# Optimization experiments

Measured on AMD Instinct MI355X. Metric: run time of the kernel, lower is better.

## Reference

```python
import jax, jax.numpy as jnp
import numpy as np

TOP_K = 2


def setup_inputs() -> dict:
    key = jax.random.key(0)
    ks = jax.random.split(key, 6)
    B, T, H, E, F = 2, 2048, 1024, 8, 4096
    s1 = 1.0 / np.sqrt(H)
    s2 = 1.0 / np.sqrt(F)
    return {
        "hidden_states": jax.random.normal(ks[0], (B, T, H), dtype=jnp.float32),
        "router_w": jax.random.normal(ks[1], (E, H), dtype=jnp.float32) * s1,
        "w1": jax.random.normal(ks[2], (E, H, F), dtype=jnp.float32) * s1,
        "b1": jnp.zeros((E, F), dtype=jnp.float32),
        "w2": jax.random.normal(ks[3], (E, F, H), dtype=jnp.float32) * s2,
        "b2": jnp.zeros((E, H), dtype=jnp.float32),
    }


def reference(hidden_states, router_w, w1, b1, w2, b2):
    # hidden_states: [B,T,H]; router_w: [E,H]; w1: [E,H,F]; w2: [E,F,H]
    E = router_w.shape[0]
    K = TOP_K
    dt = hidden_states.dtype

    # Router
    router_logits = jnp.einsum("bth,eh->bte", hidden_states, router_w)  # [B,T,E]
    topk_values, topk_indices = jax.lax.top_k(router_logits, K)         # [B,T,K]
    topk_weights = jax.nn.softmax(topk_values.astype(jnp.float32), axis=-1).astype(dt)

    # Dense all-expert MLP (module computes every expert on every token)
    h_mid = jax.nn.gelu(
        jnp.einsum("bth,ehf->btef", hidden_states, w1) + b1, approximate=False
    )  # [B,T,E,F]
    expert_outputs = jnp.einsum("btef,efh->bteh", h_mid, w2) + b2  # [B,T,E,H]

    # Gather top-K expert outputs and combine
    topk_out = jnp.take_along_axis(expert_outputs, topk_indices[..., None], axis=2)  # [B,T,K,H]
    mixed_output = jnp.sum(topk_out * topk_weights[..., None], axis=2)  # [B,T,H]

    # Load-balancing aux loss
    router_probs = jax.nn.softmax(router_logits.astype(jnp.float32), axis=-1)
    P = router_probs.mean(axis=(0, 1))                       # [E]
    hard = jax.nn.one_hot(topk_indices, E, dtype=jnp.float32)  # [B,T,K,E]
    f = hard.mean(axis=(0, 1, 2))                            # [E]
    aux_loss = jnp.float32(E) * jnp.sum(f * P)

    # concept_mat is None in a fresh module -> statement loss is exactly 0
    statement_loss = jnp.float32(0.0)
    return mixed_output, aux_loss, statement_loss
```

## Files before the change

### kernel.cpp

```cpp
#include <hip/hip_runtime.h>


typedef unsigned short ushort_t;
typedef __attribute__((ext_vector_type(2))) float f32x2;
typedef __attribute__((ext_vector_type(4))) unsigned int u32x4;
typedef __attribute__((ext_vector_type(4))) unsigned short u16x4;
typedef __attribute__((ext_vector_type(4))) float f32x4;
typedef __attribute__((ext_vector_type(8))) __bf16 bf16x8;

#define NTOK 4096
#define HD   1024
#define FD   4096
#define NE   8
#define NKTOT 8192

__device__ __forceinline__ ushort_t f2bf(float f) {
  unsigned u = __builtin_bit_cast(unsigned, f);
  u += 0x7fffu + ((u >> 16) & 1u);
  return (ushort_t)(u >> 16);
}
__device__ __forceinline__ unsigned pk2(float a, float b) {
  unsigned r;
  asm("v_cvt_pk_bf16_f32 %0, %1, %2" : "=v"(r) : "v"(a), "v"(b));
  return r;
}
__device__ __forceinline__ float bf2f(ushort_t u) {
  unsigned v = ((unsigned)u) << 16;
  return __builtin_bit_cast(float, v);
}
__device__ __forceinline__ bf16x8 frag_ld(const void* p) {
  u32x4 v = *reinterpret_cast<const u32x4*>(p);
  return __builtin_bit_cast(bf16x8, v);
}

#define GLOAD16(g, l) __builtin_amdgcn_global_load_lds(                         \
    (const __attribute__((address_space(1))) unsigned int*)(g),                 \
    (__attribute__((address_space(3))) unsigned int*)(l), 16, 0, 0)

#define WAITLGKM() do { asm volatile("s_waitcnt lgkmcnt(0)" ::: "memory");      \
                        __builtin_amdgcn_sched_barrier(0); } while (0)
#define WAITVM0()  asm volatile("s_waitcnt vmcnt(0)" ::: "memory")
#define BARRIER() do { asm volatile("s_waitcnt lgkmcnt(0)" ::: "memory");       \
                       __builtin_amdgcn_s_barrier(); } while (0)

__global__ void init_k(int* counts) {
  if (threadIdx.x < NE) counts[threadIdx.x] = 0;
}

__global__ void convx_k(const float* __restrict__ src, ushort_t* __restrict__ dst) {
  const size_t i = ((size_t)blockIdx.x * 256 + threadIdx.x) * 4;
  const f32x4 v = *reinterpret_cast<const f32x4*>(src + i);
  u16x4 o;
  o.x = f2bf(v.x); o.y = f2bf(v.y); o.z = f2bf(v.z); o.w = f2bf(v.w);
  *reinterpret_cast<u16x4*>(dst + i) = o;
}

__global__ void router_k(const float* __restrict__ x, const float* __restrict__ rw,
                         float* __restrict__ tokP, int* __restrict__ counts,
                         int* __restrict__ tk_e, int* __restrict__ tk_s,
                         float* __restrict__ tk_w) {
  const int w = threadIdx.x >> 6, l = threadIdx.x & 63;
  const int t = blockIdx.x * 4 + w;
  const float* xr = x + (size_t)t * HD;
  float acc[NE];
#pragma unroll
  for (int e = 0; e < NE; ++e) acc[e] = 0.f;
  for (int it = 0; it < HD / 64; ++it) {
    const int h = l + it * 64;
    const float xv = xr[h];
#pragma unroll
    for (int e = 0; e < NE; ++e) acc[e] = fmaf(xv, rw[e * HD + h], acc[e]);
  }
#pragma unroll
  for (int e = 0; e < NE; ++e) {
#pragma unroll
    for (int s = 32; s > 0; s >>= 1) acc[e] += __shfl_xor(acc[e], s, 64);
  }
  float m = acc[0];
#pragma unroll
  for (int e = 1; e < NE; ++e) m = fmaxf(m, acc[e]);
  float ssum = 0.f;
  float p[NE];
#pragma unroll
  for (int e = 0; e < NE; ++e) { p[e] = expf(acc[e] - m); ssum += p[e]; }
  const float inv = 1.f / ssum;
  if (l < NE) tokP[(size_t)t * NE + l] = p[l] * inv;

  if (l == 0) {
    int i0 = 0; float v0 = acc[0];
#pragma unroll
    for (int e = 1; e < NE; ++e) if (acc[e] > v0) { v0 = acc[e]; i0 = e; }
    int i1 = -1; float v1 = -3.4e38f;
#pragma unroll
    for (int e = 0; e < NE; ++e) if (e != i0 && acc[e] > v1) { v1 = acc[e]; i1 = e; }
    const float w0 = 1.f / (1.f + expf(v1 - v0));
    const int s0 = atomicAdd(&counts[i0], 1);
    const int s1 = atomicAdd(&counts[i1], 1);
    tk_e[2 * t] = i0;     tk_s[2 * t] = s0;     tk_w[2 * t] = w0;
    tk_e[2 * t + 1] = i1; tk_s[2 * t + 1] = s1; tk_w[2 * t + 1] = 1.f - w0;
  }
}

__global__ void finalize_k(const float* __restrict__ tokP, const int* __restrict__ counts,
                           int* __restrict__ offsets, float* __restrict__ out_tail) {
  __shared__ float red[16][8];
  const int tid = threadIdx.x;
  f32x4 a0 = {0.f, 0.f, 0.f, 0.f}, a1 = {0.f, 0.f, 0.f, 0.f};
#pragma unroll
  for (int k = 0; k < 4; ++k) {
    const float* p = tokP + ((size_t)tid * 4 + k) * 8;
    a0 += *reinterpret_cast<const f32x4*>(p);
    a1 += *reinterpret_cast<const f32x4*>(p + 4);
  }
#pragma unroll
  for (int s = 1; s < 64; s <<= 1) {
#pragma unroll
    for (int c = 0; c < 4; ++c) {
      a0[c] += __shfl_xor(a0[c], s, 64);
      a1[c] += __shfl_xor(a1[c], s, 64);
    }
  }
  if ((tid & 63) == 0) {
    const int wv = tid >> 6;
#pragma unroll
    for (int c = 0; c < 4; ++c) { red[wv][c] = a0[c]; red[wv][4 + c] = a1[c]; }
  }
  __syncthreads();
  if (tid == 0) {
    float P[8];
    for (int c = 0; c < 8; ++c) {
      float s = 0.f;
      for (int q = 0; q < 16; ++q) s += red[q][c];
      P[c] = s * (1.f / NTOK);
    }
    int off = 0; float aux = 0.f;
    for (int q = 0; q < NE; ++q) { offsets[q] = off; off += counts[q]; }
    for (int q = 0; q < NE; ++q) aux += ((float)counts[q] / (float)NKTOT) * P[q];
    out_tail[0] = (float)NE * aux;
    out_tail[1] = 0.f;
  }
}

__global__ void build_slots_k(const int* __restrict__ tk_e, const int* __restrict__ tk_s,
                              const int* __restrict__ offsets, int* __restrict__ slot_token) {
  const int i = blockIdx.x * 256 + threadIdx.x;
  const int e = tk_e[i];
  slot_token[offsets[e] + tk_s[i]] = i >> 1;
}

template <bool IS_G1>
__global__ __launch_bounds__(256, 4) void moe_fused(
    const ushort_t* __restrict__ A, const float* __restrict__ W,
    const float* __restrict__ bias,
    const int* __restrict__ counts, const int* __restrict__ offsets,
    const int* __restrict__ slot_token,
    ushort_t* __restrict__ midout, ushort_t* __restrict__ ybuf) {
  constexpr int KDF = IS_G1 ? HD : FD;
  constexpr int WST = IS_G1 ? FD : HD;
  constexpr int NSTEP = IS_G1 ? 16 : 32;
  const int id = blockIdx.x;
  const int e = id & 7;
  const int q = id >> 3;
  const int ty = q % 10;
  const int r = q / 10;
  const int np = IS_G1 ? r : (r >> 1);
  const int ks = IS_G1 ? 0 : (r & 1);
  const int n0 = np * 128;
  const int KB = ks * 2048;
  const int cnt = counts[e];
  if (ty * 128 >= cnt) return;
  const int off = offsets[e];
  const int pos0 = off + ty * 128;
  const int rr = cnt - ty * 128;
  const int rows_rem = rr < 128 ? rr : 128;

  __shared__ __align__(16) ushort_t lds[16384];

  const int tid = threadIdx.x;
  const int w = tid >> 6, l = tid & 63;
  const int wr = w >> 1, wc = w & 1;

  const int sw = (((l & 7) ^ ((l >> 3) & 7)) << 4);
  const char* ab[4];
#pragma unroll
  for (int c = 0; c < 4; ++c) {
    const int row = c * 32 + w * 8 + (l >> 3);
    int pos = pos0 + row; if (pos > NKTOT - 1) pos = NKTOT - 1;
    const size_t ar = IS_G1 ? (size_t)slot_token[pos] : (size_t)pos;
    ab[c] = (const char*)A + (ar * KDF + KB) * 2 + sw;
  }

  const float* wB = W + (size_t)e * ((size_t)HD * FD) +
                    ((size_t)KB + 16 * w) * WST + n0 + 2 * l;

  f32x4 acc[4][4] = {};

  for (int t = 0; t < NSTEP; ++t) {
#pragma unroll
    for (int c = 0; c < 4; ++c)
      GLOAD16(ab[c] + t * 128, &lds[(c * 32 + w * 8) * 64]);
    f32x2 R[16];
    const float* p = wB + (size_t)(t * 64) * WST;
#pragma unroll
    for (int i = 0; i < 16; ++i)
      R[i] = *reinterpret_cast<const f32x2*>(p + (size_t)i * WST);
    WAITVM0();
    {
      ushort_t* d = &lds[8192 + (2 * l) * 64];
      const int k7 = l & 7;
      u32x4 v;
      v.x = pk2(R[0].x, R[1].x); v.y = pk2(R[2].x, R[3].x);
      v.z = pk2(R[4].x, R[5].x); v.w = pk2(R[6].x, R[7].x);
      *reinterpret_cast<u32x4*>(d + (((2 * w) ^ k7) << 3)) = v;
      v.x = pk2(R[8].x, R[9].x);  v.y = pk2(R[10].x, R[11].x);
      v.z = pk2(R[12].x, R[13].x); v.w = pk2(R[14].x, R[15].x);
      *reinterpret_cast<u32x4*>(d + (((2 * w + 1) ^ k7) << 3)) = v;
      ushort_t* d2 = d + 64;
      v.x = pk2(R[0].y, R[1].y); v.y = pk2(R[2].y, R[3].y);
      v.z = pk2(R[4].y, R[5].y); v.w = pk2(R[6].y, R[7].y);
      *reinterpret_cast<u32x4*>(d2 + (((2 * w) ^ k7) << 3)) = v;
      v.x = pk2(R[8].y, R[9].y);  v.y = pk2(R[10].y, R[11].y);
      v.z = pk2(R[12].y, R[13].y); v.w = pk2(R[14].y, R[15].y);
      *reinterpret_cast<u32x4*>(d2 + (((2 * w + 1) ^ k7) << 3)) = v;
    }
    BARRIER();
    {
      const int arow = wr * 64 + (l & 15);
      const int brow = wc * 64 + (l & 15);
      const int ax = l & 7;
      const int bx = (l >> 1) & 7;
      bf16x8 afr[4], bfr[4];
#pragma unroll
      for (int kk = 0; kk < 2; ++kk) {
        const int kc = kk * 4 + (l >> 4);
#pragma unroll
        for (int mm = 0; mm < 4; ++mm)
          afr[mm] = frag_ld(&lds[(arow + mm * 16) * 64 + ((kc ^ ax) << 3)]);
#pragma unroll
        for (int nn = 0; nn < 4; ++nn)
          bfr[nn] = frag_ld(&lds[8192 + (brow + nn * 16) * 64 + ((kc ^ bx) << 3)]);
        WAITLGKM();
        __builtin_amdgcn_s_setprio(1);
#pragma unroll
        for (int mm = 0; mm < 4; ++mm)
#pragma unroll
          for (int nn = 0; nn < 4; ++nn)
            acc[mm][nn] = __builtin_amdgcn_mfma_f32_16x16x32_bf16(
                afr[mm], bfr[nn], acc[mm][nn], 0, 0, 0);
        __builtin_amdgcn_s_setprio(0);
      }
    }
    BARRIER();
  }

  {
    const int lr4 = (l >> 4) * 4, lc = l & 15;
#pragma unroll
    for (int nn = 0; nn < 4; ++nn) {
      const int col = wc * 64 + nn * 16 + lc;
      const float bv = IS_G1 ? bias[(size_t)e * FD + n0 + col] : 0.f;
#pragma unroll
      for (int mm = 0; mm < 4; ++mm) {
        const int rb = wr * 64 + mm * 16 + lr4;
#pragma unroll
        for (int j = 0; j < 4; ++j) {
          float v = acc[mm][nn][j] + bv;
          if (IS_G1) v = 0.5f * v * (1.0f + erff(v * 0.70710678118654752f));
          lds[(rb + j) * 128 + col] = f2bf(v);
        }
      }
    }
    BARRIER();
#pragma unroll
    for (int p = 0; p < 8; ++p) {
      const int idx = p * 2048 + tid * 8;
      const int row = idx >> 7;
      const int col = idx & 127;
      if (row < rows_rem) {
        const u32x4 v = *reinterpret_cast<const u32x4*>(&lds[idx]);
        if (IS_G1)
          *reinterpret_cast<u32x4*>(&midout[(size_t)(pos0 + row) * FD + n0 + col]) = v;
        else
          *reinterpret_cast<u32x4*>(
              &ybuf[((size_t)ks * NKTOT + pos0 + row) * HD + n0 + col]) = v;
      }
    }
  }
}

__global__ void combine_k(const ushort_t* __restrict__ ybuf, const int* __restrict__ tk_e,
                          const int* __restrict__ tk_s, const float* __restrict__ tk_w,
                          const int* __restrict__ offsets, const float* __restrict__ b2,
                          float* __restrict__ out) {
  const int t = blockIdx.x;
  const int e0 = tk_e[2 * t], e1 = tk_e[2 * t + 1];
  const size_t p0 = (size_t)offsets[e0] + tk_s[2 * t];
  const size_t p1 = (size_t)offsets[e1] + tk_s[2 * t + 1];
  const float w0 = tk_w[2 * t], w1v = tk_w[2 * t + 1];
  const int h = threadIdx.x * 4;
  f32x4 s0 = *reinterpret_cast<const f32x4*>(b2 + (size_t)e0 * HD + h);
  f32x4 s1 = *reinterpret_cast<const f32x4*>(b2 + (size_t)e1 * HD + h);
#pragma unroll
  for (int ks = 0; ks < 2; ++ks) {
    const u16x4 a = *reinterpret_cast<const u16x4*>(
        &ybuf[((size_t)ks * NKTOT + p0) * HD + h]);
    const u16x4 b = *reinterpret_cast<const u16x4*>(
        &ybuf[((size_t)ks * NKTOT + p1) * HD + h]);
    s0.x += bf2f(a.x); s0.y += bf2f(a.y); s0.z += bf2f(a.z); s0.w += bf2f(a.w);
    s1.x += bf2f(b.x); s1.y += bf2f(b.y); s1.z += bf2f(b.z); s1.w += bf2f(b.w);
  }
  f32x4 o = s0 * w0 + s1 * w1v;
  *reinterpret_cast<f32x4*>(out + (size_t)t * HD + h) = o;
}

extern "C" void kernel_launch(void* const* d_in, const int* in_sizes, int n_in,
                              void* d_out, int out_size, void* d_ws, size_t ws_size,
                              hipStream_t stream) {
  const float* x  = (const float*)d_in[0];
  const float* rw = (const float*)d_in[1];
  const float* w1 = (const float*)d_in[2];
  const float* b1 = (const float*)d_in[3];
  const float* w2 = (const float*)d_in[4];
  const float* b2 = (const float*)d_in[5];
  float* out = (float*)d_out;

  char* ws = (char*)d_ws;
  ushort_t* Xbf  = (ushort_t*)(ws + 0);
  ushort_t* midb = (ushort_t*)(ws + 8388608);
  ushort_t* ybuf = (ushort_t*)(ws + 75497472);
  char* sm = ws + 209715200;
  int*   counts  = (int*)(sm);
  int*   offsets = (int*)(sm + 64);
  float* tokP    = (float*)(sm + 128);
  int*   tk_e    = (int*)(sm + 128 + 131072);
  int*   tk_s    = (int*)(sm + 128 + 131072 + 32768);
  float* tk_w    = (float*)(sm + 128 + 131072 + 65536);
  int*   slot_token = (int*)(sm + 128 + 131072 + 98304);

  init_k<<<1, 64, 0, stream>>>(counts);
  convx_k<<<4096, 256, 0, stream>>>(x, Xbf);
  router_k<<<1024, 256, 0, stream>>>(x, rw, tokP, counts, tk_e, tk_s, tk_w);
  finalize_k<<<1, 1024, 0, stream>>>(tokP, counts, offsets, out + (size_t)NTOK * HD);
  build_slots_k<<<32, 256, 0, stream>>>(tk_e, tk_s, offsets, slot_token);
  moe_fused<true><<<2560, 256, 0, stream>>>(
      Xbf, w1, b1, counts, offsets, slot_token, midb, (ushort_t*)nullptr);
  moe_fused<false><<<1280, 256, 0, stream>>>(
      midb, w2, b2, counts, offsets, slot_token, (ushort_t*)nullptr, ybuf);
  combine_k<<<4096, 256, 0, stream>>>(ybuf, tk_e, tk_s, tk_w, offsets, b2, out);
}
```

Measured before the change: 463.3 us.

## Double-buffer A tiles and prefetch next K-step in larger 256-row expert GEMM blocks

Raises the expert GEMM block to 512 threads covering 256 token rows by 128 columns, which halves the grid and doubles reuse of each converted fp32 weight tile. The A tile is double-buffered in LDS, and the next step's A copy (global_load_lds) and weight register loads are issued before the MFMA compute of the current step. This overlaps memory latency with matrix math instead of stalling on vmcnt(0) each iteration. In exchange, LDS use grows to 80KB per block, which limits blocks per CU. Grouped experts with fewer tokens also waste more rows in partially filled 256-row tiles.

```diff
diff --git a/kernel.cpp b/kernel.cpp
--- a/kernel.cpp
+++ b/kernel.cpp
@@ -37,8 +37,7 @@
     (const __attribute__((address_space(1))) unsigned int*)(g),                 \
     (__attribute__((address_space(3))) unsigned int*)(l), 16, 0, 0)
 
-#define WAITLGKM() do { asm volatile("s_waitcnt lgkmcnt(0)" ::: "memory");      \
-                        __builtin_amdgcn_sched_barrier(0); } while (0)
+#define WAITVM4()  asm volatile("s_waitcnt vmcnt(4)" ::: "memory")
 #define WAITVM0()  asm volatile("s_waitcnt vmcnt(0)" ::: "memory")
 #define BARRIER() do { asm volatile("s_waitcnt lgkmcnt(0)" ::: "memory");       \
                        __builtin_amdgcn_s_barrier(); } while (0)
@@ -149,7 +148,7 @@
 }
 
 template <bool IS_G1>
-__global__ __launch_bounds__(256, 4) void moe_fused(
+__global__ __launch_bounds__(512, 4) void moe_fused(
     const ushort_t* __restrict__ A, const float* __restrict__ W,
     const float* __restrict__ bias,
     const int* __restrict__ counts, const int* __restrict__ offsets,
@@ -161,20 +160,20 @@
   const int id = blockIdx.x;
   const int e = id & 7;
   const int q = id >> 3;
-  const int ty = q % 10;
-  const int r = q / 10;
+  const int ty = q % 5;
+  const int r = q / 5;
   const int np = IS_G1 ? r : (r >> 1);
   const int ks = IS_G1 ? 0 : (r & 1);
   const int n0 = np * 128;
   const int KB = ks * 2048;
   const int cnt = counts[e];
-  if (ty * 128 >= cnt) return;
+  if (ty * 256 >= cnt) return;
   const int off = offsets[e];
-  const int pos0 = off + ty * 128;
-  const int rr = cnt - ty * 128;
-  const int rows_rem = rr < 128 ? rr : 128;
-
-  __shared__ __align__(16) ushort_t lds[16384];
+  const int pos0 = off + ty * 256;
+  const int rr = cnt - ty * 256;
+  const int rows_rem = rr < 256 ? rr : 256;
+
+  __shared__ __align__(16) ushort_t lds[40960];
 
   const int tid = threadIdx.x;
   const int w = tid >> 6, l = tid & 63;
@@ -184,74 +183,87 @@
   const char* ab[4];
 #pragma unroll
   for (int c = 0; c < 4; ++c) {
-    const int row = c * 32 + w * 8 + (l >> 3);
+    const int row = c * 64 + w * 8 + (l >> 3);
     int pos = pos0 + row; if (pos > NKTOT - 1) pos = NKTOT - 1;
     const size_t ar = IS_G1 ? (size_t)slot_token[pos] : (size_t)pos;
     ab[c] = (const char*)A + (ar * KDF + KB) * 2 + sw;
   }
 
   const float* wB = W + (size_t)e * ((size_t)HD * FD) +
-                    ((size_t)KB + 16 * w) * WST + n0 + 2 * l;
+                    ((size_t)KB + 8 * w) * WST + n0 + 2 * l;
 
   f32x4 acc[4][4] = {};
-
-  for (int t = 0; t < NSTEP; ++t) {
+  f32x2 R[8];
+
+  auto stageA = [&](int tt) {
+    const int bb = tt & 1;
 #pragma unroll
     for (int c = 0; c < 4; ++c)
-      GLOAD16(ab[c] + t * 128, &lds[(c * 32 + w * 8) * 64]);
-    f32x2 R[16];
-    const float* p = wB + (size_t)(t * 64) * WST;
-#pragma unroll
-    for (int i = 0; i < 16; ++i)
+      GLOAD16(ab[c] + tt * 128, &lds[bb * 16384 + (c * 64 + w * 8) * 64]);
+  };
+  auto issueB = [&](int tt) {
+    const float* p = wB + (size_t)tt * 64 * WST;
+#pragma unroll
+    for (int i = 0; i < 8; ++i)
       R[i] = *reinterpret_cast<const f32x2*>(p + (size_t)i * WST);
+  };
+  auto writeB = [&]() {
+    ushort_t* d = &lds[32768 + (2 * l) * 64 + ((w ^ (l & 7)) << 3)];
+    u32x4 v;
+    v.x = pk2(R[0].x, R[1].x); v.y = pk2(R[2].x, R[3].x);
+    v.z = pk2(R[4].x, R[5].x); v.w = pk2(R[6].x, R[7].x);
+    *reinterpret_cast<u32x4*>(d) = v;
+    v.x = pk2(R[0].y, R[1].y); v.y = pk2(R[2].y, R[3].y);
+    v.z = pk2(R[4].y, R[5].y); v.w = pk2(R[6].y, R[7].y);
+    *reinterpret_cast<u32x4*>(d + 64) = v;
+  };
+  auto compute = [&](int tt) {
+    const ushort_t* Ab = &lds[(tt & 1) * 16384];
+    const ushort_t* Bb = &lds[32768];
+    const int arow = wr * 64 + (l & 15);
+    const int brow = wc * 64 + (l & 15);
+    const int ax = l & 7;
+    const int bx = (l >> 1) & 7;
+    __builtin_amdgcn_s_setprio(1);
+#pragma unroll
+    for (int kk = 0; kk < 2; ++kk) {
+      const int kc = kk * 4 + (l >> 4);
+      bf16x8 afr[4];
+#pragma unroll
+      for (int mm = 0; mm < 4; ++mm)
+        afr[mm] = frag_ld(&Ab[(arow + mm * 16) * 64 + ((kc ^ ax) << 3)]);
+#pragma unroll
+      for (int nn = 0; nn < 4; ++nn) {
+        const bf16x8 bfr = frag_ld(&Bb[(brow + nn * 16) * 64 + ((kc ^ bx) << 3)]);
+#pragma unroll
+        for (int mm = 0; mm < 4; ++mm)
+          acc[mm][nn] = __builtin_amdgcn_mfma_f32_16x16x32_bf16(
+              afr[mm], bfr, acc[mm][nn], 0, 0, 0);
+      }
+    }
+    __builtin_amdgcn_s_setprio(0);
+  };
+
+  issueB(0);
+  stageA(0);
+  WAITVM4();
+  writeB();
+  WAITVM0();
+  BARRIER();
+
+  for (int t = 0; t < NSTEP - 1; ++t) {
+    issueB(t + 1);
+    stageA(t + 1);
+    __builtin_amdgcn_sched_barrier(0);
+    compute(t);
+    __builtin_amdgcn_s_barrier();
+    WAITVM4();
+    writeB();
     WAITVM0();
-    {
-      ushort_t* d = &lds[8192 + (2 * l) * 64];
-      const int k7 = l & 7;
-      u32x4 v;
-      v.x = pk2(R[0].x, R[1].x); v.y = pk2(R[2].x, R[3].x);
-      v.z = pk2(R[4].x, R[5].x); v.w = pk2(R[6].x, R[7].x);
-      *reinterpret_cast<u32x4*>(d + (((2 * w) ^ k7) << 3)) = v;
-      v.x = pk2(R[8].x, R[9].x);  v.y = pk2(R[10].x, R[11].x);
-      v.z = pk2(R[12].x, R[13].x); v.w = pk2(R[14].x, R[15].x);
-      *reinterpret_cast<u32x4*>(d + (((2 * w + 1) ^ k7) << 3)) = v;
-      ushort_t* d2 = d + 64;
-      v.x = pk2(R[0].y, R[1].y); v.y = pk2(R[2].y, R[3].y);
-      v.z = pk2(R[4].y, R[5].y); v.w = pk2(R[6].y, R[7].y);
-      *reinterpret_cast<u32x4*>(d2 + (((2 * w) ^ k7) << 3)) = v;
-      v.x = pk2(R[8].y, R[9].y);  v.y = pk2(R[10].y, R[11].y);
-      v.z = pk2(R[12].y, R[13].y); v.w = pk2(R[14].y, R[15].y);
-      *reinterpret_cast<u32x4*>(d2 + (((2 * w + 1) ^ k7) << 3)) = v;
-    }
     BARRIER();
-    {
-      const int arow = wr * 64 + (l & 15);
-      const int brow = wc * 64 + (l & 15);
-      const int ax = l & 7;
-      const int bx = (l >> 1) & 7;
-      bf16x8 afr[4], bfr[4];
-#pragma unroll
-      for (int kk = 0; kk < 2; ++kk) {
-        const int kc = kk * 4 + (l >> 4);
-#pragma unroll
-        for (int mm = 0; mm < 4; ++mm)
-          afr[mm] = frag_ld(&lds[(arow + mm * 16) * 64 + ((kc ^ ax) << 3)]);
-#pragma unroll
-        for (int nn = 0; nn < 4; ++nn)
-          bfr[nn] = frag_ld(&lds[8192 + (brow + nn * 16) * 64 + ((kc ^ bx) << 3)]);
-        WAITLGKM();
-        __builtin_amdgcn_s_setprio(1);
-#pragma unroll
-        for (int mm = 0; mm < 4; ++mm)
-#pragma unroll
-          for (int nn = 0; nn < 4; ++nn)
-            acc[mm][nn] = __builtin_amdgcn_mfma_f32_16x16x32_bf16(
-                afr[mm], bfr[nn], acc[mm][nn], 0, 0, 0);
-        __builtin_amdgcn_s_setprio(0);
-      }
-    }
-    BARRIER();
-  }
+  }
+  compute(NSTEP - 1);
+  __builtin_amdgcn_s_barrier();
 
   {
     const int lr4 = (l >> 4) * 4, lc = l & 15;
@@ -273,7 +285,7 @@
     BARRIER();
 #pragma unroll
     for (int p = 0; p < 8; ++p) {
-      const int idx = p * 2048 + tid * 8;
+      const int idx = p * 4096 + tid * 8;
       const int row = idx >> 7;
       const int col = idx & 127;
       if (row < rows_rem) {
@@ -342,9 +354,9 @@
   router_k<<<1024, 256, 0, stream>>>(x, rw, tokP, counts, tk_e, tk_s, tk_w);
   finalize_k<<<1, 1024, 0, stream>>>(tokP, counts, offsets, out + (size_t)NTOK * HD);
   build_slots_k<<<32, 256, 0, stream>>>(tk_e, tk_s, offsets, slot_token);
-  moe_fused<true><<<2560, 256, 0, stream>>>(
+  moe_fused<true><<<1280, 512, 0, stream>>>(
       Xbf, w1, b1, counts, offsets, slot_token, midb, (ushort_t*)nullptr);
-  moe_fused<false><<<1280, 256, 0, stream>>>(
+  moe_fused<false><<<640, 512, 0, stream>>>(
       midb, w2, b2, counts, offsets, slot_token, (ushort_t*)nullptr, ybuf);
   combine_k<<<4096, 256, 0, stream>>>(ybuf, tk_e, tk_s, tk_w, offsets, b2, out);
 }
```

New measurement: 397.8 us. 14.1% less time.

## Software-pipeline MoE GEMM loads, raise second-GEMM split-K, fuse bf16 cast into router

Applied to the files above, without the earlier changes.

Restructures the expert GEMM main loop as a multi-stage pipeline. Activation tiles are triple-buffered in LDS. Weight tiles are prefetched two steps ahead into alternating register sets, with partial vmcnt waits, and double-buffered in LDS. This is meant to hide global-load latency behind MFMA work. The second GEMM's split-K goes from 2 to 4 with twice as many blocks, and combine_k now sums four partials. The separate fp32-to-bf16 conversion kernel is folded into the router pass. The larger LDS footprint and the occupancy hint dropped to 2 blocks per CU reduce concurrency. The extra split-K partials add more ybuf traffic in combine.

```diff
diff --git a/kernel.cpp b/kernel.cpp
--- a/kernel.cpp
+++ b/kernel.cpp
@@ -37,9 +37,7 @@
     (const __attribute__((address_space(1))) unsigned int*)(g),                 \
     (__attribute__((address_space(3))) unsigned int*)(l), 16, 0, 0)
 
-#define WAITLGKM() do { asm volatile("s_waitcnt lgkmcnt(0)" ::: "memory");      \
-                        __builtin_amdgcn_sched_barrier(0); } while (0)
-#define WAITVM0()  asm volatile("s_waitcnt vmcnt(0)" ::: "memory")
+#define WAITVM(N) asm volatile("s_waitcnt vmcnt(" #N ")" ::: "memory")
 #define BARRIER() do { asm volatile("s_waitcnt lgkmcnt(0)" ::: "memory");       \
                        __builtin_amdgcn_s_barrier(); } while (0)
 
@@ -47,27 +45,22 @@
   if (threadIdx.x < NE) counts[threadIdx.x] = 0;
 }
 
-__global__ void convx_k(const float* __restrict__ src, ushort_t* __restrict__ dst) {
-  const size_t i = ((size_t)blockIdx.x * 256 + threadIdx.x) * 4;
-  const f32x4 v = *reinterpret_cast<const f32x4*>(src + i);
-  u16x4 o;
-  o.x = f2bf(v.x); o.y = f2bf(v.y); o.z = f2bf(v.z); o.w = f2bf(v.w);
-  *reinterpret_cast<u16x4*>(dst + i) = o;
-}
-
 __global__ void router_k(const float* __restrict__ x, const float* __restrict__ rw,
+                         ushort_t* __restrict__ Xbf,
                          float* __restrict__ tokP, int* __restrict__ counts,
                          int* __restrict__ tk_e, int* __restrict__ tk_s,
                          float* __restrict__ tk_w) {
   const int w = threadIdx.x >> 6, l = threadIdx.x & 63;
   const int t = blockIdx.x * 4 + w;
   const float* xr = x + (size_t)t * HD;
+  ushort_t* xo = Xbf + (size_t)t * HD;
   float acc[NE];
 #pragma unroll
   for (int e = 0; e < NE; ++e) acc[e] = 0.f;
   for (int it = 0; it < HD / 64; ++it) {
     const int h = l + it * 64;
     const float xv = xr[h];
+    xo[h] = f2bf(xv);
 #pragma unroll
     for (int e = 0; e < NE; ++e) acc[e] = fmaf(xv, rw[e * HD + h], acc[e]);
   }
@@ -149,7 +142,7 @@
 }
 
 template <bool IS_G1>
-__global__ __launch_bounds__(256, 4) void moe_fused(
+__global__ __launch_bounds__(256, 2) void moe_fused(
     const ushort_t* __restrict__ A, const float* __restrict__ W,
     const float* __restrict__ bias,
     const int* __restrict__ counts, const int* __restrict__ offsets,
@@ -157,16 +150,15 @@
     ushort_t* __restrict__ midout, ushort_t* __restrict__ ybuf) {
   constexpr int KDF = IS_G1 ? HD : FD;
   constexpr int WST = IS_G1 ? FD : HD;
-  constexpr int NSTEP = IS_G1 ? 16 : 32;
   const int id = blockIdx.x;
   const int e = id & 7;
   const int q = id >> 3;
   const int ty = q % 10;
   const int r = q / 10;
-  const int np = IS_G1 ? r : (r >> 1);
-  const int ks = IS_G1 ? 0 : (r & 1);
+  const int np = IS_G1 ? r : (r >> 2);
+  const int ks = IS_G1 ? 0 : (r & 3);
   const int n0 = np * 128;
-  const int KB = ks * 2048;
+  const int KB = ks * 1024;
   const int cnt = counts[e];
   if (ty * 128 >= cnt) return;
   const int off = offsets[e];
@@ -174,7 +166,7 @@
   const int rr = cnt - ty * 128;
   const int rows_rem = rr < 128 ? rr : 128;
 
-  __shared__ __align__(16) ushort_t lds[16384];
+  __shared__ __align__(16) ushort_t lds[40960];
 
   const int tid = threadIdx.x;
   const int w = tid >> 6, l = tid & 63;
@@ -194,62 +186,84 @@
                     ((size_t)KB + 16 * w) * WST + n0 + 2 * l;
 
   f32x4 acc[4][4] = {};
-
-  for (int t = 0; t < NSTEP; ++t) {
+  f32x2 R0[16], R1[16];
+
+  auto stageA = [&](int tt, int buf) {
 #pragma unroll
     for (int c = 0; c < 4; ++c)
-      GLOAD16(ab[c] + t * 128, &lds[(c * 32 + w * 8) * 64]);
-    f32x2 R[16];
-    const float* p = wB + (size_t)(t * 64) * WST;
+      GLOAD16(ab[c] + tt * 128, &lds[buf * 8192 + (c * 32 + w * 8) * 64]);
+  };
+  auto issueB = [&](int tt, f32x2 (&R)[16]) {
+    const float* p = wB + (size_t)tt * 64 * WST;
 #pragma unroll
     for (int i = 0; i < 16; ++i)
       R[i] = *reinterpret_cast<const f32x2*>(p + (size_t)i * WST);
-    WAITVM0();
-    {
-      ushort_t* d = &lds[8192 + (2 * l) * 64];
-      const int k7 = l & 7;
-      u32x4 v;
-      v.x = pk2(R[0].x, R[1].x); v.y = pk2(R[2].x, R[3].x);
-      v.z = pk2(R[4].x, R[5].x); v.w = pk2(R[6].x, R[7].x);
-      *reinterpret_cast<u32x4*>(d + (((2 * w) ^ k7) << 3)) = v;
-      v.x = pk2(R[8].x, R[9].x);  v.y = pk2(R[10].x, R[11].x);
-      v.z = pk2(R[12].x, R[13].x); v.w = pk2(R[14].x, R[15].x);
-      *reinterpret_cast<u32x4*>(d + (((2 * w + 1) ^ k7) << 3)) = v;
-      ushort_t* d2 = d + 64;
-      v.x = pk2(R[0].y, R[1].y); v.y = pk2(R[2].y, R[3].y);
-      v.z = pk2(R[4].y, R[5].y); v.w = pk2(R[6].y, R[7].y);
-      *reinterpret_cast<u32x4*>(d2 + (((2 * w) ^ k7) << 3)) = v;
-      v.x = pk2(R[8].y, R[9].y);  v.y = pk2(R[10].y, R[11].y);
-      v.z = pk2(R[12].y, R[13].y); v.w = pk2(R[14].y, R[15].y);
-      *reinterpret_cast<u32x4*>(d2 + (((2 * w + 1) ^ k7) << 3)) = v;
-    }
-    BARRIER();
-    {
-      const int arow = wr * 64 + (l & 15);
-      const int brow = wc * 64 + (l & 15);
-      const int ax = l & 7;
-      const int bx = (l >> 1) & 7;
-      bf16x8 afr[4], bfr[4];
-#pragma unroll
-      for (int kk = 0; kk < 2; ++kk) {
-        const int kc = kk * 4 + (l >> 4);
+  };
+  auto writeB = [&](int buf, const f32x2 (&R)[16]) {
+    const int key = l & 7;
+    ushort_t* d = &lds[24576 + buf * 8192 + (2 * l) * 64];
+    u32x4 v;
+    v.x = pk2(R[0].x, R[1].x);   v.y = pk2(R[2].x, R[3].x);
+    v.z = pk2(R[4].x, R[5].x);   v.w = pk2(R[6].x, R[7].x);
+    *reinterpret_cast<u32x4*>(d + (((2 * w) ^ key) << 3)) = v;
+    v.x = pk2(R[8].x, R[9].x);   v.y = pk2(R[10].x, R[11].x);
+    v.z = pk2(R[12].x, R[13].x); v.w = pk2(R[14].x, R[15].x);
+    *reinterpret_cast<u32x4*>(d + (((2 * w + 1) ^ key) << 3)) = v;
+    ushort_t* d2 = d + 64;
+    v.x = pk2(R[0].y, R[1].y);   v.y = pk2(R[2].y, R[3].y);
+    v.z = pk2(R[4].y, R[5].y);   v.w = pk2(R[6].y, R[7].y);
+    *reinterpret_cast<u32x4*>(d2 + (((2 * w) ^ key) << 3)) = v;
+    v.x = pk2(R[8].y, R[9].y);   v.y = pk2(R[10].y, R[11].y);
+    v.z = pk2(R[12].y, R[13].y); v.w = pk2(R[14].y, R[15].y);
+    *reinterpret_cast<u32x4*>(d2 + (((2 * w + 1) ^ key) << 3)) = v;
+  };
+  auto compute = [&](int abuf, int bbuf) {
+    const ushort_t* Ab = &lds[abuf * 8192];
+    const ushort_t* Bb = &lds[24576 + bbuf * 8192];
+    const int arow = wr * 64 + (l & 15);
+    const int brow = wc * 64 + (l & 15);
+    const int ax = l & 7;
+    const int bx = (l >> 1) & 7;
+#pragma unroll
+    for (int kk = 0; kk < 2; ++kk) {
+      const int kc = kk * 4 + (l >> 4);
+      bf16x8 afr[4];
+#pragma unroll
+      for (int mm = 0; mm < 4; ++mm)
+        afr[mm] = frag_ld(&Ab[(arow + mm * 16) * 64 + ((kc ^ ax) << 3)]);
+      __builtin_amdgcn_s_setprio(1);
+#pragma unroll
+      for (int nn = 0; nn < 4; ++nn) {
+        const bf16x8 bfr = frag_ld(&Bb[(brow + nn * 16) * 64 + ((kc ^ bx) << 3)]);
 #pragma unroll
         for (int mm = 0; mm < 4; ++mm)
-          afr[mm] = frag_ld(&lds[(arow + mm * 16) * 64 + ((kc ^ ax) << 3)]);
-#pragma unroll
-        for (int nn = 0; nn < 4; ++nn)
-          bfr[nn] = frag_ld(&lds[8192 + (brow + nn * 16) * 64 + ((kc ^ bx) << 3)]);
-        WAITLGKM();
-        __builtin_amdgcn_s_setprio(1);
-#pragma unroll
-        for (int mm = 0; mm < 4; ++mm)
-#pragma unroll
-          for (int nn = 0; nn < 4; ++nn)
-            acc[mm][nn] = __builtin_amdgcn_mfma_f32_16x16x32_bf16(
-                afr[mm], bfr[nn], acc[mm][nn], 0, 0, 0);
-        __builtin_amdgcn_s_setprio(0);
+          acc[mm][nn] = __builtin_amdgcn_mfma_f32_16x16x32_bf16(
+              afr[mm], bfr, acc[mm][nn], 0, 0, 0);
       }
-    }
+      __builtin_amdgcn_s_setprio(0);
+    }
+  };
+
+  stageA(0, 0);
+  stageA(1, 1);
+  issueB(0, R0);
+  issueB(1, R1);
+  WAITVM(16);
+  writeB(0, R0);
+  BARRIER();
+
+#pragma unroll
+  for (int t = 0; t < 16; ++t) {
+    if (t <= 13) { if (t & 1) issueB(t + 2, R1); else issueB(t + 2, R0); }
+    if (t == 0)       { WAITVM(16); }
+    else if (t <= 13) { WAITVM(20); }
+    else if (t == 14) { WAITVM(4);  }
+    if (t <= 14) { if (t & 1) writeB((t + 1) & 1, R0); else writeB((t + 1) & 1, R1); }
+    if (t <= 13) stageA(t + 2, (t + 2) % 3);
+    __builtin_amdgcn_sched_barrier(0);
+    compute(t % 3, t & 1);
+    if (t >= 1 && t <= 13) { WAITVM(20); }
+    else if (t == 14)      { WAITVM(0);  }
     BARRIER();
   }
 
@@ -301,7 +315,7 @@
   f32x4 s0 = *reinterpret_cast<const f32x4*>(b2 + (size_t)e0 * HD + h);
   f32x4 s1 = *reinterpret_cast<const f32x4*>(b2 + (size_t)e1 * HD + h);
 #pragma unroll
-  for (int ks = 0; ks < 2; ++ks) {
+  for (int ks = 0; ks < 4; ++ks) {
     const u16x4 a = *reinterpret_cast<const u16x4*>(
         &ybuf[((size_t)ks * NKTOT + p0) * HD + h]);
     const u16x4 b = *reinterpret_cast<const u16x4*>(
@@ -338,13 +352,12 @@
   int*   slot_token = (int*)(sm + 128 + 131072 + 98304);
 
   init_k<<<1, 64, 0, stream>>>(counts);
-  convx_k<<<4096, 256, 0, stream>>>(x, Xbf);
-  router_k<<<1024, 256, 0, stream>>>(x, rw, tokP, counts, tk_e, tk_s, tk_w);
+  router_k<<<1024, 256, 0, stream>>>(x, rw, Xbf, tokP, counts, tk_e, tk_s, tk_w);
   finalize_k<<<1, 1024, 0, stream>>>(tokP, counts, offsets, out + (size_t)NTOK * HD);
   build_slots_k<<<32, 256, 0, stream>>>(tk_e, tk_s, offsets, slot_token);
   moe_fused<true><<<2560, 256, 0, stream>>>(
       Xbf, w1, b1, counts, offsets, slot_token, midb, (ushort_t*)nullptr);
-  moe_fused<false><<<1280, 256, 0, stream>>>(
+  moe_fused<false><<<2560, 256, 0, stream>>>(
       midb, w2, b2, counts, offsets, slot_token, (ushort_t*)nullptr, ybuf);
   combine_k<<<4096, 256, 0, stream>>>(ybuf, tk_e, tk_s, tk_w, offsets, b2, out);
 }
```

Result: slower. 500.0 us (+7.9%).

## Keep expert weight slices resident in LDS and loop blocks over token tiles

Applied to the files above, without the earlier changes.

Each block of both expert GEMMs now converts its fp32 weight slice to bf16 once into a large shared-memory buffer, then loops over all token tiles of its expert. Before, every token tile re-streamed and re-converted the fp32 weights. The down-projection switches to an 8-way K split, so the combine step now sums eight bf16 partials. The separate bf16 cast of x is folded into the router kernel. The trade-off is about 144KB of LDS per block (one block per CU), a grid of only 512 blocks open to per-expert load imbalance, and eight times more partial-output traffic.

```diff
diff --git a/kernel.cpp b/kernel.cpp
--- a/kernel.cpp
+++ b/kernel.cpp
@@ -2,7 +2,6 @@
 
 
 typedef unsigned short ushort_t;
-typedef __attribute__((ext_vector_type(2))) float f32x2;
 typedef __attribute__((ext_vector_type(4))) unsigned int u32x4;
 typedef __attribute__((ext_vector_type(4))) unsigned short u16x4;
 typedef __attribute__((ext_vector_type(4))) float f32x4;
@@ -19,11 +18,6 @@
   u += 0x7fffu + ((u >> 16) & 1u);
   return (ushort_t)(u >> 16);
 }
-__device__ __forceinline__ unsigned pk2(float a, float b) {
-  unsigned r;
-  asm("v_cvt_pk_bf16_f32 %0, %1, %2" : "=v"(r) : "v"(a), "v"(b));
-  return r;
-}
 __device__ __forceinline__ float bf2f(ushort_t u) {
   unsigned v = ((unsigned)u) << 16;
   return __builtin_bit_cast(float, v);
@@ -33,13 +27,7 @@
   return __builtin_bit_cast(bf16x8, v);
 }
 
-#define GLOAD16(g, l) __builtin_amdgcn_global_load_lds(                         \
-    (const __attribute__((address_space(1))) unsigned int*)(g),                 \
-    (__attribute__((address_space(3))) unsigned int*)(l), 16, 0, 0)
-
-#define WAITLGKM() do { asm volatile("s_waitcnt lgkmcnt(0)" ::: "memory");      \
-                        __builtin_amdgcn_sched_barrier(0); } while (0)
-#define WAITVM0()  asm volatile("s_waitcnt vmcnt(0)" ::: "memory")
+#define WAITVM0() asm volatile("s_waitcnt vmcnt(0)" ::: "memory")
 #define BARRIER() do { asm volatile("s_waitcnt lgkmcnt(0)" ::: "memory");       \
                        __builtin_amdgcn_s_barrier(); } while (0)
 
@@ -47,27 +35,22 @@
   if (threadIdx.x < NE) counts[threadIdx.x] = 0;
 }
 
-__global__ void convx_k(const float* __restrict__ src, ushort_t* __restrict__ dst) {
-  const size_t i = ((size_t)blockIdx.x * 256 + threadIdx.x) * 4;
-  const f32x4 v = *reinterpret_cast<const f32x4*>(src + i);
-  u16x4 o;
-  o.x = f2bf(v.x); o.y = f2bf(v.y); o.z = f2bf(v.z); o.w = f2bf(v.w);
-  *reinterpret_cast<u16x4*>(dst + i) = o;
-}
-
 __global__ void router_k(const float* __restrict__ x, const float* __restrict__ rw,
+                         ushort_t* __restrict__ Xbf,
                          float* __restrict__ tokP, int* __restrict__ counts,
                          int* __restrict__ tk_e, int* __restrict__ tk_s,
                          float* __restrict__ tk_w) {
   const int w = threadIdx.x >> 6, l = threadIdx.x & 63;
   const int t = blockIdx.x * 4 + w;
   const float* xr = x + (size_t)t * HD;
+  ushort_t* xo = Xbf + (size_t)t * HD;
   float acc[NE];
 #pragma unroll
   for (int e = 0; e < NE; ++e) acc[e] = 0.f;
   for (int it = 0; it < HD / 64; ++it) {
     const int h = l + it * 64;
     const float xv = xr[h];
+    xo[h] = f2bf(xv);
 #pragma unroll
     for (int e = 0; e < NE; ++e) acc[e] = fmaf(xv, rw[e * HD + h], acc[e]);
   }
@@ -149,7 +132,7 @@
 }
 
 template <bool IS_G1>
-__global__ __launch_bounds__(256, 4) void moe_fused(
+__global__ __launch_bounds__(256) void moe_resident(
     const ushort_t* __restrict__ A, const float* __restrict__ W,
     const float* __restrict__ bias,
     const int* __restrict__ counts, const int* __restrict__ offsets,
@@ -157,132 +140,181 @@
     ushort_t* __restrict__ midout, ushort_t* __restrict__ ybuf) {
   constexpr int KDF = IS_G1 ? HD : FD;
   constexpr int WST = IS_G1 ? FD : HD;
-  constexpr int NSTEP = IS_G1 ? 16 : 32;
+  constexpr int NW  = IS_G1 ? 64 : 128;
+  constexpr int KW  = IS_G1 ? 1024 : 512;
+  constexpr int NSTEP = KW / 64;
+  constexpr int NF = IS_G1 ? 2 : 4;
   const int id = blockIdx.x;
   const int e = id & 7;
   const int q = id >> 3;
-  const int ty = q % 10;
-  const int r = q / 10;
-  const int np = IS_G1 ? r : (r >> 1);
-  const int ks = IS_G1 ? 0 : (r & 1);
-  const int n0 = np * 128;
-  const int KB = ks * 2048;
+  const int np = IS_G1 ? q : (q & 7);
+  const int ks = IS_G1 ? 0 : (q >> 3);
+  const int n0 = np * NW;
+  const int KB = ks * KW;
   const int cnt = counts[e];
-  if (ty * 128 >= cnt) return;
   const int off = offsets[e];
-  const int pos0 = off + ty * 128;
-  const int rr = cnt - ty * 128;
-  const int rows_rem = rr < 128 ? rr : 128;
-
-  __shared__ __align__(16) ushort_t lds[16384];
+  const int nty = (cnt + 127) >> 7;
+
+  __shared__ __align__(16) ushort_t Bs[NW * KW];
+  __shared__ __align__(16) ushort_t As[8192];
 
   const int tid = threadIdx.x;
+
+  {
+    constexpr int TPR = NW / 4;
+    constexpr int RPP = 256 / TPR;
+    const int kr = tid / TPR;
+    const int nc = (tid % TPR) * 4;
+    const float* src = W + (size_t)e * ((size_t)HD * FD) +
+                       (size_t)(KB + kr) * WST + n0 + nc;
+    f32x4 R[8];
+    for (int g = 0; g < KW / RPP; g += 8) {
+#pragma unroll
+      for (int j = 0; j < 8; ++j)
+        R[j] = *reinterpret_cast<const f32x4*>(src + (size_t)(g + j) * RPP * WST);
+#pragma unroll
+      for (int j = 0; j < 8; ++j) {
+        const int k = (g + j) * RPP + kr;
+#pragma unroll
+        for (int c = 0; c < 4; ++c) {
+          const int n = nc + c;
+          Bs[n * KW + (((k >> 3) ^ (n & 7)) << 3) + (k & 7)] = f2bf(R[j][c]);
+        }
+      }
+    }
+  }
+  BARRIER();
+
   const int w = tid >> 6, l = tid & 63;
   const int wr = w >> 1, wc = w & 1;
-
-  const int sw = (((l & 7) ^ ((l >> 3) & 7)) << 4);
-  const char* ab[4];
-#pragma unroll
-  for (int c = 0; c < 4; ++c) {
-    const int row = c * 32 + w * 8 + (l >> 3);
-    int pos = pos0 + row; if (pos > NKTOT - 1) pos = NKTOT - 1;
-    const size_t ar = IS_G1 ? (size_t)slot_token[pos] : (size_t)pos;
-    ab[c] = (const char*)A + (ar * KDF + KB) * 2 + sw;
-  }
-
-  const float* wB = W + (size_t)e * ((size_t)HD * FD) +
-                    ((size_t)KB + 16 * w) * WST + n0 + 2 * l;
-
-  f32x4 acc[4][4] = {};
-
-  for (int t = 0; t < NSTEP; ++t) {
-#pragma unroll
-    for (int c = 0; c < 4; ++c)
-      GLOAD16(ab[c] + t * 128, &lds[(c * 32 + w * 8) * 64]);
-    f32x2 R[16];
-    const float* p = wB + (size_t)(t * 64) * WST;
-#pragma unroll
-    for (int i = 0; i < 16; ++i)
-      R[i] = *reinterpret_cast<const f32x2*>(p + (size_t)i * WST);
+  const int key = l & 7;
+
+  f32x4 acc[4][NF];
+  u32x4 RA[4];
+
+  auto writeA = [&]() {
+#pragma unroll
+    for (int c = 0; c < 4; ++c) {
+      const int row = c * 32 + w * 8 + (l >> 3);
+      *reinterpret_cast<u32x4*>(&As[row * 64 + (((l & 7) ^ (row & 7)) << 3)]) = RA[c];
+    }
+  };
+
+  for (int ty = 0; ty < nty; ++ty) {
+    const int pos0 = off + ty * 128;
+    const int rr = cnt - ty * 128;
+    const int rows_rem = rr < 128 ? rr : 128;
+
+    const char* ab[4];
+#pragma unroll
+    for (int c = 0; c < 4; ++c) {
+      const int row = c * 32 + w * 8 + (l >> 3);
+      int pos = pos0 + row; if (pos > NKTOT - 1) pos = NKTOT - 1;
+      const size_t ar = IS_G1 ? (size_t)slot_token[pos] : (size_t)pos;
+      ab[c] = (const char*)A + (ar * KDF + KB) * 2 + (l & 7) * 16;
+    }
+#pragma unroll
+    for (int mm = 0; mm < 4; ++mm)
+#pragma unroll
+      for (int nn = 0; nn < NF; ++nn) acc[mm][nn] = f32x4{0.f, 0.f, 0.f, 0.f};
+
+#pragma unroll
+    for (int c = 0; c < 4; ++c) RA[c] = *reinterpret_cast<const u32x4*>(ab[c]);
     WAITVM0();
-    {
-      ushort_t* d = &lds[8192 + (2 * l) * 64];
-      const int k7 = l & 7;
-      u32x4 v;
-      v.x = pk2(R[0].x, R[1].x); v.y = pk2(R[2].x, R[3].x);
-      v.z = pk2(R[4].x, R[5].x); v.w = pk2(R[6].x, R[7].x);
-      *reinterpret_cast<u32x4*>(d + (((2 * w) ^ k7) << 3)) = v;
-      v.x = pk2(R[8].x, R[9].x);  v.y = pk2(R[10].x, R[11].x);
-      v.z = pk2(R[12].x, R[13].x); v.w = pk2(R[14].x, R[15].x);
-      *reinterpret_cast<u32x4*>(d + (((2 * w + 1) ^ k7) << 3)) = v;
-      ushort_t* d2 = d + 64;
-      v.x = pk2(R[0].y, R[1].y); v.y = pk2(R[2].y, R[3].y);
-      v.z = pk2(R[4].y, R[5].y); v.w = pk2(R[6].y, R[7].y);
-      *reinterpret_cast<u32x4*>(d2 + (((2 * w) ^ k7) << 3)) = v;
-      v.x = pk2(R[8].y, R[9].y);  v.y = pk2(R[10].y, R[11].y);
-      v.z = pk2(R[12].y, R[13].y); v.w = pk2(R[14].y, R[15].y);
-      *reinterpret_cast<u32x4*>(d2 + (((2 * w + 1) ^ k7) << 3)) = v;
-    }
+    writeA();
     BARRIER();
-    {
-      const int arow = wr * 64 + (l & 15);
-      const int brow = wc * 64 + (l & 15);
-      const int ax = l & 7;
-      const int bx = (l >> 1) & 7;
-      bf16x8 afr[4], bfr[4];
-#pragma unroll
-      for (int kk = 0; kk < 2; ++kk) {
-        const int kc = kk * 4 + (l >> 4);
-#pragma unroll
-        for (int mm = 0; mm < 4; ++mm)
-          afr[mm] = frag_ld(&lds[(arow + mm * 16) * 64 + ((kc ^ ax) << 3)]);
-#pragma unroll
-        for (int nn = 0; nn < 4; ++nn)
-          bfr[nn] = frag_ld(&lds[8192 + (brow + nn * 16) * 64 + ((kc ^ bx) << 3)]);
-        WAITLGKM();
-        __builtin_amdgcn_s_setprio(1);
-#pragma unroll
-        for (int mm = 0; mm < 4; ++mm)
-#pragma unroll
-          for (int nn = 0; nn < 4; ++nn)
-            acc[mm][nn] = __builtin_amdgcn_mfma_f32_16x16x32_bf16(
-                afr[mm], bfr[nn], acc[mm][nn], 0, 0, 0);
-        __builtin_amdgcn_s_setprio(0);
-      }
-    }
-    BARRIER();
-  }
-
-  {
+
+    for (int t = 0; t < NSTEP; ++t) {
+      if (t + 1 < NSTEP) {
+#pragma unroll
+        for (int c = 0; c < 4; ++c)
+          RA[c] = *reinterpret_cast<const u32x4*>(ab[c] + (t + 1) * 128);
+      }
+      __builtin_amdgcn_sched_barrier(0);
+      {
+        const int arow = wr * 64 + (l & 15);
+        const int brow = wc * (NW / 2) + (l & 15);
+#pragma unroll
+        for (int kk = 0; kk < 2; ++kk) {
+          const int kcA = kk * 4 + (l >> 4);
+          const int kcB = t * 8 + kcA;
+          bf16x8 afr[4];
+#pragma unroll
+          for (int mm = 0; mm < 4; ++mm)
+            afr[mm] = frag_ld(&As[(arow + mm * 16) * 64 + ((kcA ^ key) << 3)]);
+          __builtin_amdgcn_s_setprio(1);
+#pragma unroll
+          for (int nn = 0; nn < NF; ++nn) {
+            const bf16x8 bfr =
+                frag_ld(&Bs[(brow + nn * 16) * KW + ((kcB ^ key) << 3)]);
+#pragma unroll
+            for (int mm = 0; mm < 4; ++mm)
+              acc[mm][nn] = __builtin_amdgcn_mfma_f32_16x16x32_bf16(
+                  afr[mm], bfr, acc[mm][nn], 0, 0, 0);
+          }
+          __builtin_amdgcn_s_setprio(0);
+        }
+      }
+      __builtin_amdgcn_s_barrier();
+      if (t + 1 < NSTEP) { WAITVM0(); writeA(); }
+      BARRIER();
+    }
+
     const int lr4 = (l >> 4) * 4, lc = l & 15;
-#pragma unroll
-    for (int nn = 0; nn < 4; ++nn) {
-      const int col = wc * 64 + nn * 16 + lc;
-      const float bv = IS_G1 ? bias[(size_t)e * FD + n0 + col] : 0.f;
-#pragma unroll
-      for (int mm = 0; mm < 4; ++mm) {
-        const int rb = wr * 64 + mm * 16 + lr4;
-#pragma unroll
-        for (int j = 0; j < 4; ++j) {
-          float v = acc[mm][nn][j] + bv;
-          if (IS_G1) v = 0.5f * v * (1.0f + erff(v * 0.70710678118654752f));
-          lds[(rb + j) * 128 + col] = f2bf(v);
-        }
-      }
-    }
-    BARRIER();
-#pragma unroll
-    for (int p = 0; p < 8; ++p) {
-      const int idx = p * 2048 + tid * 8;
-      const int row = idx >> 7;
-      const int col = idx & 127;
-      if (row < rows_rem) {
-        const u32x4 v = *reinterpret_cast<const u32x4*>(&lds[idx]);
-        if (IS_G1)
-          *reinterpret_cast<u32x4*>(&midout[(size_t)(pos0 + row) * FD + n0 + col]) = v;
-        else
-          *reinterpret_cast<u32x4*>(
-              &ybuf[((size_t)ks * NKTOT + pos0 + row) * HD + n0 + col]) = v;
+    if (IS_G1) {
+#pragma unroll
+      for (int nn = 0; nn < NF; ++nn) {
+        const int col = wc * 32 + nn * 16 + lc;
+        const float bv = bias[(size_t)e * FD + n0 + col];
+#pragma unroll
+        for (int mm = 0; mm < 4; ++mm) {
+          const int rb = wr * 64 + mm * 16 + lr4;
+#pragma unroll
+          for (int j = 0; j < 4; ++j) {
+            float v = acc[mm][nn][j] + bv;
+            v = 0.5f * v * (1.0f + erff(v * 0.70710678118654752f));
+            As[(rb + j) * 64 + col] = f2bf(v);
+          }
+        }
+      }
+      BARRIER();
+#pragma unroll
+      for (int p = 0; p < 4; ++p) {
+        const int idx = p * 2048 + tid * 8;
+        const int row = idx >> 6, col = idx & 63;
+        if (row < rows_rem)
+          *reinterpret_cast<u32x4*>(&midout[(size_t)(pos0 + row) * FD + n0 + col]) =
+              *reinterpret_cast<const u32x4*>(&As[idx]);
+      }
+      BARRIER();
+    } else {
+#pragma unroll
+      for (int h = 0; h < 2; ++h) {
+        if (wr == h) {
+#pragma unroll
+          for (int nn = 0; nn < 4; ++nn) {
+            const int col = wc * 64 + nn * 16 + lc;
+#pragma unroll
+            for (int mm = 0; mm < 4; ++mm) {
+              const int rbl = mm * 16 + lr4;
+#pragma unroll
+              for (int j = 0; j < 4; ++j)
+                As[(rbl + j) * 128 + col] = f2bf(acc[mm][nn][j]);
+            }
+          }
+        }
+        BARRIER();
+#pragma unroll
+        for (int p = 0; p < 4; ++p) {
+          const int idx = p * 2048 + tid * 8;
+          const int rowl = idx >> 7, col = idx & 127;
+          const int row = h * 64 + rowl;
+          if (row < rows_rem)
+            *reinterpret_cast<u32x4*>(
+                &ybuf[((size_t)ks * NKTOT + pos0 + row) * HD + n0 + col]) =
+                *reinterpret_cast<const u32x4*>(&As[idx]);
+        }
+        BARRIER();
       }
     }
   }
@@ -301,7 +333,7 @@
   f32x4 s0 = *reinterpret_cast<const f32x4*>(b2 + (size_t)e0 * HD + h);
   f32x4 s1 = *reinterpret_cast<const f32x4*>(b2 + (size_t)e1 * HD + h);
 #pragma unroll
-  for (int ks = 0; ks < 2; ++ks) {
+  for (int ks = 0; ks < 8; ++ks) {
     const u16x4 a = *reinterpret_cast<const u16x4*>(
         &ybuf[((size_t)ks * NKTOT + p0) * HD + h]);
     const u16x4 b = *reinterpret_cast<const u16x4*>(
@@ -338,13 +370,12 @@
   int*   slot_token = (int*)(sm + 128 + 131072 + 98304);
 
   init_k<<<1, 64, 0, stream>>>(counts);
-  convx_k<<<4096, 256, 0, stream>>>(x, Xbf);
-  router_k<<<1024, 256, 0, stream>>>(x, rw, tokP, counts, tk_e, tk_s, tk_w);
+  router_k<<<1024, 256, 0, stream>>>(x, rw, Xbf, tokP, counts, tk_e, tk_s, tk_w);
   finalize_k<<<1, 1024, 0, stream>>>(tokP, counts, offsets, out + (size_t)NTOK * HD);
   build_slots_k<<<32, 256, 0, stream>>>(tk_e, tk_s, offsets, slot_token);
-  moe_fused<true><<<2560, 256, 0, stream>>>(
+  moe_resident<true><<<512, 256, 0, stream>>>(
       Xbf, w1, b1, counts, offsets, slot_token, midb, (ushort_t*)nullptr);
-  moe_fused<false><<<1280, 256, 0, stream>>>(
+  moe_resident<false><<<512, 256, 0, stream>>>(
       midb, w2, b2, counts, offsets, slot_token, (ushort_t*)nullptr, ybuf);
   combine_k<<<4096, 256, 0, stream>>>(ybuf, tk_e, tk_s, tk_w, offsets, b2, out);
 }
```

Result: slower. 575.2 us (+24.2%).
